# Optimization experiments

Hardware: AMD Instinct MI355X
Metric: run time of the kernel (lower is better)

Reference implementation:

```python
import jax, jax.numpy as jnp
import numpy as np

NH, NKV, HD, PD = 16, 4, 128, 16  # heads, kv heads, head dim, rotary partial dim
BASE = 10000.0
QK_GAIN_INIT = 5.25


def _rms_norm(x):
    # F.rms_norm over last dim, eps = dtype eps (torch default when eps=None)
    return x * jax.lax.rsqrt(jnp.mean(x * x, axis=-1, keepdims=True) + jnp.finfo(x.dtype).eps)


def _rope_partial(x, cos, sin):
    # rotate first PD dims (two halves of PD//2), pass through the rest
    h = PD // 2
    x1, x2, xp = x[..., :h], x[..., h:PD], x[..., PD:]
    return jnp.concatenate([x1 * cos + x2 * sin, -x2 * cos + x1 * sin, xp], axis=-1)


def setup_inputs() -> dict:
    key = jax.random.key(0)
    ks = jax.random.split(key, 5)
    B, T, D = 2, 2048, 2048
    KD = NKV * HD
    s = 0.02
    return {
        "x": jax.random.normal(ks[0], (B, T, D), jnp.float32),
        "wq": jax.random.normal(ks[1], (D, D), jnp.float32) * s,
        "wk": jax.random.normal(ks[2], (KD, D), jnp.float32) * s,
        "wv": jax.random.normal(ks[3], (KD, D), jnp.float32) * s,
        "wp": jax.random.normal(ks[4], (D, D), jnp.float32) * s,
        "qg": jnp.full((NH,), QK_GAIN_INIT, jnp.float32),
    }


def reference(x, wq, wk, wv, wp, qg):
    B, T, D = x.shape
    q = (x @ wq.T).reshape(B, T, NH, HD)    # [B,T,NH,HD]
    k = (x @ wk.T).reshape(B, T, NKV, HD)   # [B,T,NKV,HD]
    v = (x @ wv.T).reshape(B, T, NKV, HD)
    q = _rms_norm(q)
    k = _rms_norm(k)
    # partial rotary tables: [T, PD//2] -> broadcast over head dim
    t = jnp.arange(T, dtype=jnp.float32)
    inv = 1.0 / (BASE ** (jnp.arange(0, PD, 2, dtype=jnp.float32) / PD))
    f = t[:, None] * inv[None, :]
    cos, sin = jnp.cos(f)[:, None, :], jnp.sin(f)[:, None, :]  # [T,1,PD//2]
    q = _rope_partial(q, cos, sin)
    k = _rope_partial(k, cos, sin)
    q = q * qg[None, None, :, None]         # learned per-head QK gain
    scale = 1.0 / jnp.sqrt(jnp.float32(HD))
    G = NH // NKV
    qh = q.reshape(B, T, NKV, G, HD)
    scores = jnp.einsum('bqkgd,bskd->bkgqs', qh, k) * scale  # [B,NKV,G,T,T]
    causal = jnp.arange(T)[:, None] >= jnp.arange(T)[None, :]
    scores = jnp.where(causal[None, None, None], scores, -jnp.inf)
    p = jax.nn.softmax(scores, axis=-1)
    y = jnp.einsum('bkgqs,bskd->bqkgd', p, v).reshape(B, T, D)
    return y @ wp.T
```

## Files before the change

### kernel.cpp

```cpp
#include <hip/hip_runtime.h>
#include <hip/hip_bf16.h>

#define B_   2
#define T_   2048
#define D_   2048
#define NH_  16
#define NKV_ 4
#define HD_  128
#define KD_  512
#define BT_  4096

typedef __bf16 bf16x8 __attribute__((ext_vector_type(8)));
typedef float  f32x4  __attribute__((ext_vector_type(4)));
typedef float  f32x16 __attribute__((ext_vector_type(16)));

__device__ __forceinline__ void gload_lds16(const __hip_bfloat16* g, __hip_bfloat16* l) {
    __builtin_amdgcn_global_load_lds(
        (__attribute__((address_space(1))) void*)(g),
        (__attribute__((address_space(3))) void*)(l),
        16, 0, 0);
}

__global__ void f2b_all(const float4* __restrict__ x,  const float4* __restrict__ wq,
                        const float4* __restrict__ wk, const float4* __restrict__ wv,
                        const float4* __restrict__ wp,
                        ushort4* __restrict__ xb,  ushort4* __restrict__ wqb,
                        ushort4* __restrict__ wkb, ushort4* __restrict__ wvb,
                        ushort4* __restrict__ wpb) {
    const int e0 = BT_ * D_ / 4;
    const int e1 = e0 + D_ * D_ / 4;
    const int e2 = e1 + KD_ * D_ / 4;
    const int e3 = e2 + KD_ * D_ / 4;
    const int e4 = e3 + D_ * D_ / 4;
    int idx = blockIdx.x * blockDim.x + threadIdx.x;
    int stride = gridDim.x * blockDim.x;
    for (int j = idx; j < e4; j += stride) {
        const float4* src; ushort4* dst; int off;
        if      (j < e0) { src = x;  dst = xb;  off = j; }
        else if (j < e1) { src = wq; dst = wqb; off = j - e0; }
        else if (j < e2) { src = wk; dst = wkb; off = j - e1; }
        else if (j < e3) { src = wv; dst = wvb; off = j - e2; }
        else             { src = wp; dst = wpb; off = j - e3; }
        float4 v = src[off];
        __hip_bfloat16 a = __float2bfloat16(v.x), b = __float2bfloat16(v.y),
                       c = __float2bfloat16(v.z), d = __float2bfloat16(v.w);
        ushort4 o;
        o.x = *(const unsigned short*)&a; o.y = *(const unsigned short*)&b;
        o.z = *(const unsigned short*)&c; o.w = *(const unsigned short*)&d;
        dst[off] = o;
    }
}

#define GEMM_TILE_BODY(Aptr, Bptr, Cptr, colL, Nc, K)                                         \
    const int tid = threadIdx.x, w = tid >> 6, lane = tid & 63;                               \
    const int lr = lane & 15, lk = lane >> 4;                                                 \
    const int wr = w >> 1, wc = w & 1;                                                        \
    const size_t row0 = (size_t)blockIdx.x * 128;                                             \
    const __hip_bfloat16* ga = (Aptr) + (row0 + tid / 4) * (K) + (tid % 4) * 8;               \
    const __hip_bfloat16* gb = (Bptr) + ((size_t)(colL) + tid / 4) * (K) + (tid % 4) * 8;     \
    const int KI = (K) >> 5;                                                                  \
    auto stage = [&](int u) {                                                                 \
        int uu = u < KI ? u : KI - 1;                                                         \
        const int kk = uu * 32;                                                               \
        const int slot = u & 3;                                                               \
        gload_lds16(ga + kk,                  &As[slot][w * 512]);                            \
        gload_lds16(ga + kk + (size_t)64*(K), &As[slot][2048 + w * 512]);                     \
        gload_lds16(gb + kk,                  &Bs[slot][w * 512]);                            \
        gload_lds16(gb + kk + (size_t)64*(K), &Bs[slot][2048 + w * 512]);                     \
    };                                                                                        \
    f32x4 acc[4][4] = {};                                                                     \
    stage(0); stage(1);                                                                       \
    for (int kt = 0; kt < KI; ++kt) {                                                         \
        stage(kt + 2);                                                                        \
        asm volatile("s_waitcnt vmcnt(8)" ::: "memory");                                      \
        __builtin_amdgcn_s_barrier();                                                         \
        __builtin_amdgcn_sched_barrier(0);                                                    \
        const int slot = kt & 3;                                                              \
        bf16x8 af[4], bfr[4];                                                                 \
        _Pragma("unroll")                                                                     \
        for (int m = 0; m < 4; m++)                                                           \
            af[m] = *(const bf16x8*)&As[slot][(wr * 64 + m * 16 + lr) * 32 + lk * 8];         \
        _Pragma("unroll")                                                                     \
        for (int n = 0; n < 4; n++)                                                           \
            bfr[n] = *(const bf16x8*)&Bs[slot][(wc * 64 + n * 16 + lr) * 32 + lk * 8];        \
        _Pragma("unroll")                                                                     \
        for (int m = 0; m < 4; m++)                                                           \
            _Pragma("unroll")                                                                 \
            for (int n = 0; n < 4; n++)                                                       \
                acc[m][n] = __builtin_amdgcn_mfma_f32_16x16x32_bf16(af[m], bfr[n],            \
                                                                    acc[m][n], 0, 0, 0);      \
    }                                                                                         \
    _Pragma("unroll")                                                                         \
    for (int m = 0; m < 4; m++)                                                               \
        _Pragma("unroll")                                                                     \
        for (int n = 0; n < 4; n++)                                                           \
            _Pragma("unroll")                                                                 \
            for (int r = 0; r < 4; r++)                                                       \
                (Cptr)[(row0 + wr * 64 + m * 16 + lk * 4 + r) * (Nc)                          \
                       + (colL) + wc * 64 + n * 16 + lr] = acc[m][n][r];

__global__ __launch_bounds__(256, 2)
void gemm_qkv(const __hip_bfloat16* __restrict__ A,
              const __hip_bfloat16* __restrict__ Wq, const __hip_bfloat16* __restrict__ Wk,
              const __hip_bfloat16* __restrict__ Wv,
              float* __restrict__ Cq, float* __restrict__ Ck, float* __restrict__ Cv) {
    __shared__ __attribute__((aligned(16))) __hip_bfloat16 As[4][4096];
    __shared__ __attribute__((aligned(16))) __hip_bfloat16 Bs[4][4096];
    const int cb = blockIdx.y;
    const __hip_bfloat16* Bw; float* Cm; int Nc, colL;
    if (cb < 16)      { Bw = Wq; Cm = Cq; Nc = D_;  colL = cb * 128; }
    else if (cb < 20) { Bw = Wk; Cm = Ck; Nc = KD_; colL = (cb - 16) * 128; }
    else              { Bw = Wv; Cm = Cv; Nc = KD_; colL = (cb - 20) * 128; }
    GEMM_TILE_BODY(A, Bw, Cm, colL, Nc, D_)
}

__global__ __launch_bounds__(256, 2)
void gemm_p(const __hip_bfloat16* __restrict__ A, const __hip_bfloat16* __restrict__ B,
            float* __restrict__ C, int N, int K) {
    __shared__ __attribute__((aligned(16))) __hip_bfloat16 As[4][4096];
    __shared__ __attribute__((aligned(16))) __hip_bfloat16 Bs[4][4096];
    const int colL = blockIdx.y * 128;
    GEMM_TILE_BODY(A, B, C, colL, N, K)
}

__global__ __launch_bounds__(256)
void norm_rope(const float* __restrict__ qf, const float* __restrict__ kf, const float* __restrict__ vf,
               const float* __restrict__ qg,
               __hip_bfloat16* __restrict__ qb, __hip_bfloat16* __restrict__ kfb, __hip_bfloat16* __restrict__ vb) {
    int wid  = (blockIdx.x * 256 + threadIdx.x) >> 6;
    int lane = threadIdx.x & 63;
    int bt = wid / 24, hh = wid % 24;
    int b = bt >> 11, t = bt & (T_ - 1);

    const float* row;
    if (hh < NH_)            row = qf + (size_t)bt * D_  + hh * HD_;
    else if (hh < NH_+NKV_)  row = kf + (size_t)bt * KD_ + (hh - NH_) * HD_;
    else                     row = vf + (size_t)bt * KD_ + (hh - NH_ - NKV_) * HD_;

    float2 xv = *(const float2*)(row + lane * 2);

    if (hh >= NH_ + NKV_) {
        int kv = hh - NH_ - NKV_;
        __hip_bfloat16* o = vb + ((size_t)(b * NKV_ + kv) * T_ + t) * HD_ + lane * 2;
        o[0] = __float2bfloat16(xv.x); o[1] = __float2bfloat16(xv.y);
        return;
    }

    float ss = xv.x * xv.x + xv.y * xv.y;
    #pragma unroll
    for (int off = 32; off; off >>= 1) ss += __shfl_xor(ss, off);
    float rn = rsqrtf(ss * (1.0f / HD_) + 1.1920929e-7f);
    float y0 = xv.x * rn, y1 = xv.y * rn;

    float py0 = __shfl_xor(y0, 4), py1 = __shfl_xor(y1, 4);
    float o0 = y0, o1 = y1;
    if (lane < 8) {
        int i0 = (2 * lane) & 7;
        float f0 = (float)t * exp2f(-(float)i0       * 1.66096404744368f);
        float f1 = (float)t * exp2f(-(float)(i0 + 1) * 1.66096404744368f);
        float s0, c0, s1, c1;
        sincosf(f0, &s0, &c0);
        sincosf(f1, &s1, &c1);
        if (lane < 4) { o0 =  y0 * c0 + py0 * s0; o1 =  y1 * c1 + py1 * s1; }
        else          { o0 = -y0 * c0 + py0 * s0; o1 = -y1 * c1 + py1 * s1; }
    }

    if (hh < NH_) {
        float g = qg[hh] * 0.1275174305f;
        o0 *= g; o1 *= g;
        __hip_bfloat16* o = qb + ((size_t)(b * NH_ + hh) * T_ + t) * HD_ + lane * 2;
        o[0] = __float2bfloat16(o0); o[1] = __float2bfloat16(o1);
    } else {
        int kv = hh - NH_;
        int hb  = lane >> 3;
        int hi2 = (lane >> 2) & 1;
        int j   = (2 * lane) & 7;
        size_t idxe = (size_t)(b * NKV_ + kv) * T_ * HD_
                    + (size_t)((((t >> 5) * 8 + hb) * 2 + hi2)) * 256 + (t & 31) * 8 + j;
        __hip_bfloat16* o = kfb + idxe;
        o[0] = __float2bfloat16(o0); o[1] = __float2bfloat16(o1);
    }
}

__global__ void vfrag_k(const __hip_bfloat16* __restrict__ vb, __hip_bfloat16* __restrict__ vfb) {
    __shared__ __hip_bfloat16 tile[32][33];
    int bk = blockIdx.z;
    int t0 = blockIdx.x * 32, d0 = blockIdx.y * 32;
    int tx = threadIdx.x, ty = threadIdx.y;
    const __hip_bfloat16* src = vb + ((size_t)bk * T_ + t0) * HD_ + d0;
    #pragma unroll
    for (int j = 0; j < 4; j++) tile[ty + j * 8][tx] = src[(size_t)(ty + j * 8) * HD_ + tx];
    __syncthreads();
    if (ty < 4) {
        int sect = ty, l31 = tx;
        ushort4 u0, u1;
        unsigned short* up0 = (unsigned short*)&u0;
        unsigned short* up1 = (unsigned short*)&u1;
        #pragma unroll
        for (int j = 0; j < 4; j++) up0[j] = *(const unsigned short*)&tile[sect * 8 + j][l31];
        #pragma unroll
        for (int j = 0; j < 4; j++) up1[j] = *(const unsigned short*)&tile[sect * 8 + 4 + j][l31];
        ushort4* dst = (ushort4*)(vfb + (size_t)bk * T_ * HD_
                     + (size_t)((((blockIdx.x * 4 + blockIdx.y) * 4 + sect) * 32 + l31)) * 8);
        dst[0] = u0; dst[1] = u1;
    }
}

__device__ __forceinline__ unsigned pkbf(float a, float b) {
    __hip_bfloat16 x = __float2bfloat16(a), y = __float2bfloat16(b);
    unsigned short xu = *(const unsigned short*)&x, yu = *(const unsigned short*)&y;
    return (unsigned)xu | ((unsigned)yu << 16);
}

union U8u { unsigned u[4]; bf16x8 v; };

__global__ __launch_bounds__(512, 2)
void attn_fwd(const __hip_bfloat16* __restrict__ qb, const __hip_bfloat16* __restrict__ kfb,
              const __hip_bfloat16* __restrict__ vfb, __hip_bfloat16* __restrict__ yb) {
    __shared__ float Mrg[4][4224];
    const int tid  = threadIdx.x;
    const int w    = tid >> 6, lane = tid & 63;
    const int l31  = lane & 31, hi = lane >> 5;
    const int hd4  = w & 3;
    const int seg  = w >> 2;
    const int bid  = blockIdx.x;
    const int strm = bid & 7;
    const int b    = strm >> 2, kvh = strm & 3;
    const int idx  = bid >> 3;
    const int c    = (idx < 32) ? (63 - 2 * idx) : (126 - 2 * idx);
    const int ns   = (c >> 1) + 1;
    const int h    = kvh * 4 + hd4;
    const int qa   = c * 32;

    const __hip_bfloat16* qp  = qb  + ((size_t)(b * NH_ + h) * T_ + qa) * HD_;
    const __hip_bfloat16* kfp = kfb + (size_t)(b * NKV_ + kvh) * T_ * HD_ + lane * 8;
    const __hip_bfloat16* vfp = vfb + (size_t)(b * NKV_ + kvh) * T_ * HD_ + lane * 8;

    bf16x8 qfr[8];
    #pragma unroll
    for (int hb = 0; hb < 8; ++hb)
        qfr[hb] = *(const bf16x8*)(qp + (size_t)l31 * HD_ + hb * 16 + hi * 8);

    f32x16 o0 = {}, o1 = {}, o2 = {}, o3 = {};
    float m = -1e30f, s = 0.f;

    bf16x8 kk[8], vv[8];
    {
        int kt0 = seg ? (ns <= c ? ns : c) : 0;
        #pragma unroll
        for (int hb = 0; hb < 8; ++hb)
            kk[hb] = *(const bf16x8*)(kfp + ((size_t)kt0 * 16 + hb * 2) * 256);
    }

    for (int t = 0; t < ns; ++t) {
        __builtin_amdgcn_s_barrier();

        const int kt_raw = seg ? ns + t : t;
        const bool dead  = kt_raw > c;
        const int kt     = dead ? c : kt_raw;

        #pragma unroll
        for (int db = 0; db < 4; ++db) {
            vv[db * 2]     = *(const bf16x8*)(vfp + ((size_t)kt * 16 + db * 4) * 256);
            vv[db * 2 + 1] = *(const bf16x8*)(vfp + ((size_t)kt * 16 + db * 4) * 256 + 512);
        }

        f32x16 sa = {};
        __builtin_amdgcn_s_setprio(1);
        #pragma unroll
        for (int hb = 0; hb < 8; ++hb)
            sa = __builtin_amdgcn_mfma_f32_32x32x16_bf16(kk[hb], qfr[hb], sa, 0, 0, 0);
        __builtin_amdgcn_s_setprio(0);

        {
            int ktn_r = (seg ? ns : 0) + t + 1;
            int ktn = ktn_r > c ? c : ktn_r;
            #pragma unroll
            for (int hb = 0; hb < 8; ++hb)
                kk[hb] = *(const bf16x8*)(kfp + ((size_t)ktn * 16 + hb * 2) * 256);
        }

        if (dead) {
            #pragma unroll
            for (int r = 0; r < 16; ++r) sa[r] = -1e30f;
        } else if (kt == c) {
            #pragma unroll
            for (int r = 0; r < 16; ++r) {
                int kvrel = (r & 3) + 8 * (r >> 2) + 4 * hi;
                if (kvrel > l31) sa[r] = -1e30f;
            }
        }
        float pm = sa[0];
        #pragma unroll
        for (int r = 1; r < 16; ++r) pm = fmaxf(pm, sa[r]);
        pm = fmaxf(pm, __shfl_xor(pm, 32));
        if (!__all(pm <= m + 8.f)) {
            float mn = fmaxf(m, pm);
            float corr = exp2f(m - mn);
            s *= corr;
            #pragma unroll
            for (int r = 0; r < 16; ++r) { o0[r] *= corr; o1[r] *= corr; o2[r] *= corr; o3[r] *= corr; }
            m = mn;
        }
        float p[16]; float rs = 0.f;
        #pragma unroll
        for (int r = 0; r < 16; ++r) { p[r] = exp2f(sa[r] - m); rs += p[r]; }
        rs += __shfl_xor(rs, 32);
        s += rs;
        unsigned pk[8];
        #pragma unroll
        for (int jj = 0; jj < 8; ++jj) pk[jj] = pkbf(p[2 * jj], p[2 * jj + 1]);
        unsigned pks[8];
        #pragma unroll
        for (int jj = 0; jj < 8; ++jj) pks[jj] = (unsigned)__shfl_xor((int)pk[jj], 32);
        U8u pa0, pa1;
        pa0.u[0] = hi ? pks[2] : pk[0];
        pa0.u[1] = hi ? pks[3] : pk[1];
        pa0.u[2] = hi ? pk[2]  : pks[0];
        pa0.u[3] = hi ? pk[3]  : pks[1];
        pa1.u[0] = hi ? pks[6] : pk[4];
        pa1.u[1] = hi ? pks[7] : pk[5];
        pa1.u[2] = hi ? pk[6]  : pks[4];
        pa1.u[3] = hi ? pk[7]  : pks[5];
        __builtin_amdgcn_s_setprio(1);
        o0 = __builtin_amdgcn_mfma_f32_32x32x16_bf16(vv[0], pa0.v, o0, 0, 0, 0);
        o0 = __builtin_amdgcn_mfma_f32_32x32x16_bf16(vv[1], pa1.v, o0, 0, 0, 0);
        o1 = __builtin_amdgcn_mfma_f32_32x32x16_bf16(vv[2], pa0.v, o1, 0, 0, 0);
        o1 = __builtin_amdgcn_mfma_f32_32x32x16_bf16(vv[3], pa1.v, o1, 0, 0, 0);
        o2 = __builtin_amdgcn_mfma_f32_32x32x16_bf16(vv[4], pa0.v, o2, 0, 0, 0);
        o2 = __builtin_amdgcn_mfma_f32_32x32x16_bf16(vv[5], pa1.v, o2, 0, 0, 0);
        o3 = __builtin_amdgcn_mfma_f32_32x32x16_bf16(vv[6], pa0.v, o3, 0, 0, 0);
        o3 = __builtin_amdgcn_mfma_f32_32x32x16_bf16(vv[7], pa1.v, o3, 0, 0, 0);
        __builtin_amdgcn_s_setprio(0);
    }

    __syncthreads();
    float* Mh = &Mrg[hd4][0];
    if (seg == 1) {
        #pragma unroll
        for (int r = 0; r < 16; ++r) {
            Mh[(0 * 16 + r) * 64 + lane] = o0[r];
            Mh[(1 * 16 + r) * 64 + lane] = o1[r];
            Mh[(2 * 16 + r) * 64 + lane] = o2[r];
            Mh[(3 * 16 + r) * 64 + lane] = o3[r];
        }
        Mh[4096 + lane] = m;
        Mh[4160 + lane] = s;
    }
    __syncthreads();
    if (seg == 0) {
        float m1 = Mh[4096 + lane], s1 = Mh[4160 + lane];
        float mn = fmaxf(m, m1);
        float ca = exp2f(m - mn), cb = exp2f(m1 - mn);
        s = s * ca + s1 * cb;
        #pragma unroll
        for (int r = 0; r < 16; ++r) {
            o0[r] = o0[r] * ca + Mh[(0 * 16 + r) * 64 + lane] * cb;
            o1[r] = o1[r] * ca + Mh[(1 * 16 + r) * 64 + lane] * cb;
            o2[r] = o2[r] * ca + Mh[(2 * 16 + r) * 64 + lane] * cb;
            o3[r] = o3[r] * ca + Mh[(3 * 16 + r) * 64 + lane] * cb;
        }
        float inv = 1.0f / s;
        __hip_bfloat16* yrow = yb + ((size_t)b * T_ + qa + l31) * D_ + h * HD_;
        #define WRITE_DB(ON, DB)                                                        \
            _Pragma("unroll")                                                           \
            for (int r4 = 0; r4 < 4; ++r4) {                                            \
                ushort4 u;                                                              \
                __hip_bfloat16 e0 = __float2bfloat16(ON[4*r4+0] * inv);                 \
                __hip_bfloat16 e1 = __float2bfloat16(ON[4*r4+1] * inv);                 \
                __hip_bfloat16 e2 = __float2bfloat16(ON[4*r4+2] * inv);                 \
                __hip_bfloat16 e3 = __float2bfloat16(ON[4*r4+3] * inv);                 \
                u.x = *(const unsigned short*)&e0; u.y = *(const unsigned short*)&e1;   \
                u.z = *(const unsigned short*)&e2; u.w = *(const unsigned short*)&e3;   \
                *(ushort4*)(yrow + (DB) * 32 + 8 * r4 + 4 * hi) = u;                    \
            }
        WRITE_DB(o0, 0) WRITE_DB(o1, 1) WRITE_DB(o2, 2) WRITE_DB(o3, 3)
        #undef WRITE_DB
    }
}

extern "C" void kernel_launch(void* const* d_in, const int* in_sizes, int n_in,
                              void* d_out, int out_size, void* d_ws, size_t ws_size,
                              hipStream_t stream) {
    (void)in_sizes; (void)n_in; (void)out_size; (void)ws_size;
    const float* x  = (const float*)d_in[0];
    const float* wq = (const float*)d_in[1];
    const float* wk = (const float*)d_in[2];
    const float* wv = (const float*)d_in[3];
    const float* wp = (const float*)d_in[4];
    const float* qg = (const float*)d_in[5];
    float* out = (float*)d_out;

    char* ws = (char*)d_ws;
    size_t off = 0;
    auto alloc = [&](size_t bytes) { char* p = ws + off; off += (bytes + 255) & ~(size_t)255; return p; };

    __hip_bfloat16* xb  = (__hip_bfloat16*)alloc((size_t)BT_ * D_ * 2);
    __hip_bfloat16* wqb = (__hip_bfloat16*)alloc((size_t)D_ * D_ * 2);
    __hip_bfloat16* wkb = (__hip_bfloat16*)alloc((size_t)KD_ * D_ * 2);
    __hip_bfloat16* wvb = (__hip_bfloat16*)alloc((size_t)KD_ * D_ * 2);
    __hip_bfloat16* wpb = (__hip_bfloat16*)alloc((size_t)D_ * D_ * 2);
    float* qf = (float*)alloc((size_t)BT_ * D_ * 4);
    float* kf = (float*)alloc((size_t)BT_ * KD_ * 4);
    float* vf = (float*)alloc((size_t)BT_ * KD_ * 4);
    __hip_bfloat16* qbb = (__hip_bfloat16*)alloc((size_t)BT_ * D_ * 2);
    __hip_bfloat16* kfb = (__hip_bfloat16*)alloc((size_t)BT_ * KD_ * 2);
    __hip_bfloat16* vfb = (__hip_bfloat16*)alloc((size_t)BT_ * KD_ * 2);
    __hip_bfloat16* ybb = xb;
    __hip_bfloat16* vbb = wqb;

    f2b_all<<<2048, 256, 0, stream>>>((const float4*)x, (const float4*)wq, (const float4*)wk,
                                      (const float4*)wv, (const float4*)wp,
                                      (ushort4*)xb, (ushort4*)wqb, (ushort4*)wkb,
                                      (ushort4*)wvb, (ushort4*)wpb);

    dim3 gqkv(BT_ / 128, 24);
    gemm_qkv<<<gqkv, 256, 0, stream>>>(xb, wqb, wkb, wvb, qf, kf, vf);

    norm_rope<<<(BT_ * 24) / 4, 256, 0, stream>>>(qf, kf, vf, qg, qbb, kfb, vbb);

    dim3 gt(T_ / 32, HD_ / 32, B_ * NKV_);
    vfrag_k<<<gt, dim3(32, 8), 0, stream>>>(vbb, vfb);

    attn_fwd<<<512, 512, 0, stream>>>(qbb, kfb, vfb, ybb);

    dim3 gq(BT_ / 128, D_ / 128);
    gemm_p<<<gq, 256, 0, stream>>>(ybb, wpb, out, D_, D_);
}
```

Before: 236.8 us.

## Split attention KV range four ways per head pair and pair query chunks

```diff
diff --git a/kernel.cpp b/kernel.cpp
--- a/kernel.cpp
+++ b/kernel.cpp
@@ -214,168 +214,183 @@
 
 union U8u { unsigned u[4]; bf16x8 v; };
 
-__global__ __launch_bounds__(512, 2)
+__global__ __launch_bounds__(512, 4)
 void attn_fwd(const __hip_bfloat16* __restrict__ qb, const __hip_bfloat16* __restrict__ kfb,
               const __hip_bfloat16* __restrict__ vfb, __hip_bfloat16* __restrict__ yb) {
-    __shared__ float Mrg[4][4224];
+    __shared__ float Mrg[2][2][4224];
     const int tid  = threadIdx.x;
     const int w    = tid >> 6, lane = tid & 63;
     const int l31  = lane & 31, hi = lane >> 5;
-    const int hd4  = w & 3;
-    const int seg  = w >> 2;
+    const int hsel = w & 1;
+    const int seg  = w >> 1;
     const int bid  = blockIdx.x;
     const int strm = bid & 7;
     const int b    = strm >> 2, kvh = strm & 3;
-    const int idx  = bid >> 3;
-    const int c    = (idx < 32) ? (63 - 2 * idx) : (126 - 2 * idx);
-    const int ns   = (c >> 1) + 1;
-    const int h    = kvh * 4 + hd4;
-    const int qa   = c * 32;
-
-    const __hip_bfloat16* qp  = qb  + ((size_t)(b * NH_ + h) * T_ + qa) * HD_;
+    const int j    = bid >> 3;
+    const int hg   = j & 1, i = j >> 1;
+    const int h    = kvh * 4 + hg * 2 + hsel;
+
     const __hip_bfloat16* kfp = kfb + (size_t)(b * NKV_ + kvh) * T_ * HD_ + lane * 8;
     const __hip_bfloat16* vfp = vfb + (size_t)(b * NKV_ + kvh) * T_ * HD_ + lane * 8;
 
-    bf16x8 qfr[8];
     #pragma unroll
-    for (int hb = 0; hb < 8; ++hb)
-        qfr[hb] = *(const bf16x8*)(qp + (size_t)l31 * HD_ + hb * 16 + hi * 8);
-
-    f32x16 o0 = {}, o1 = {}, o2 = {}, o3 = {};
-    float m = -1e30f, s = 0.f;
-
-    bf16x8 kk[8], vv[8];
-    {
-        int kt0 = seg ? (ns <= c ? ns : c) : 0;
+    for (int phase = 0; phase < 2; ++phase) {
+        const int c  = phase == 0 ? 63 - 2 * i : 2 * i;
+        const int qa = c * 32;
+        const int L  = (c >> 2) + 1;
+
+        const __hip_bfloat16* qp = qb + ((size_t)(b * NH_ + h) * T_ + qa) * HD_;
+        bf16x8 qfr[8];
         #pragma unroll
         for (int hb = 0; hb < 8; ++hb)
-            kk[hb] = *(const bf16x8*)(kfp + ((size_t)kt0 * 16 + hb * 2) * 256);
-    }
-
-    for (int t = 0; t < ns; ++t) {
-        __builtin_amdgcn_s_barrier();
-
-        const int kt_raw = seg ? ns + t : t;
-        const bool dead  = kt_raw > c;
-        const int kt     = dead ? c : kt_raw;
-
-        #pragma unroll
-        for (int db = 0; db < 4; ++db) {
-            vv[db * 2]     = *(const bf16x8*)(vfp + ((size_t)kt * 16 + db * 4) * 256);
-            vv[db * 2 + 1] = *(const bf16x8*)(vfp + ((size_t)kt * 16 + db * 4) * 256 + 512);
+            qfr[hb] = *(const bf16x8*)(qp + (size_t)l31 * HD_ + hb * 16 + hi * 8);
+
+        f32x16 o0 = {}, o1 = {}, o2 = {}, o3 = {};
+        float m = -1e30f, s = 0.f;
+
+        bf16x8 kk[8], vv[8];
+        {
+            int kt0 = seg * L; if (kt0 > c) kt0 = c;
+            #pragma unroll
+            for (int hb = 0; hb < 8; ++hb)
+                kk[hb] = *(const bf16x8*)(kfp + ((size_t)kt0 * 16 + hb * 2) * 256);
         }
 
-        f32x16 sa = {};
-        __builtin_amdgcn_s_setprio(1);
-        #pragma unroll
-        for (int hb = 0; hb < 8; ++hb)
-            sa = __builtin_amdgcn_mfma_f32_32x32x16_bf16(kk[hb], qfr[hb], sa, 0, 0, 0);
-        __builtin_amdgcn_s_setprio(0);
-
-        {
-            int ktn_r = (seg ? ns : 0) + t + 1;
-            int ktn = ktn_r > c ? c : ktn_r;
+        for (int t = 0; t < L; ++t) {
+            const int kt_raw = seg * L + t;
+            const bool dead  = kt_raw > c;
+            const int kt     = dead ? c : kt_raw;
+
+            #pragma unroll
+            for (int db = 0; db < 4; ++db) {
+                vv[db * 2]     = *(const bf16x8*)(vfp + ((size_t)kt * 16 + db * 4) * 256);
+                vv[db * 2 + 1] = *(const bf16x8*)(vfp + ((size_t)kt * 16 + db * 4) * 256 + 512);
+            }
+
+            f32x16 sa = {};
+            __builtin_amdgcn_s_setprio(1);
             #pragma unroll
             for (int hb = 0; hb < 8; ++hb)
-                kk[hb] = *(const bf16x8*)(kfp + ((size_t)ktn * 16 + hb * 2) * 256);
+                sa = __builtin_amdgcn_mfma_f32_32x32x16_bf16(kk[hb], qfr[hb], sa, 0, 0, 0);
+            __builtin_amdgcn_s_setprio(0);
+
+            {
+                int ktn = seg * L + t + 1; if (ktn > c) ktn = c;
+                #pragma unroll
+                for (int hb = 0; hb < 8; ++hb)
+                    kk[hb] = *(const bf16x8*)(kfp + ((size_t)ktn * 16 + hb * 2) * 256);
+            }
+
+            if (dead) {
+                #pragma unroll
+                for (int r = 0; r < 16; ++r) sa[r] = -1e30f;
+            } else if (kt == c) {
+                #pragma unroll
+                for (int r = 0; r < 16; ++r) {
+                    int kvrel = (r & 3) + 8 * (r >> 2) + 4 * hi;
+                    if (kvrel > l31) sa[r] = -1e30f;
+                }
+            }
+            float pm = sa[0];
+            #pragma unroll
+            for (int r = 1; r < 16; ++r) pm = fmaxf(pm, sa[r]);
+            pm = fmaxf(pm, __shfl_xor(pm, 32));
+            if (!__all(pm <= m + 8.f)) {
+                float mn = fmaxf(m, pm);
+                float corr = exp2f(m - mn);
+                s *= corr;
+                #pragma unroll
+                for (int r = 0; r < 16; ++r) { o0[r] *= corr; o1[r] *= corr; o2[r] *= corr; o3[r] *= corr; }
+                m = mn;
+            }
+            float p[16]; float rs = 0.f;
+            #pragma unroll
+            for (int r = 0; r < 16; ++r) { p[r] = exp2f(sa[r] - m); rs += p[r]; }
+            rs += __shfl_xor(rs, 32);
+            s += rs;
+            unsigned pk[8];
+            #pragma unroll
+            for (int jj = 0; jj < 8; ++jj) pk[jj] = pkbf(p[2 * jj], p[2 * jj + 1]);
+            unsigned pks[8];
+            #pragma unroll
+            for (int jj = 0; jj < 8; ++jj) pks[jj] = (unsigned)__shfl_xor((int)pk[jj], 32);
+            U8u pa0, pa1;
+            pa0.u[0] = hi ? pks[2] : pk[0];
+            pa0.u[1] = hi ? pks[3] : pk[1];
+            pa0.u[2] = hi ? pk[2]  : pks[0];
+            pa0.u[3] = hi ? pk[3]  : pks[1];
+            pa1.u[0] = hi ? pks[6] : pk[4];
+            pa1.u[1] = hi ? pks[7] : pk[5];
+            pa1.u[2] = hi ? pk[6]  : pks[4];
+            pa1.u[3] = hi ? pk[7]  : pks[5];
+            __builtin_amdgcn_s_setprio(1);
+            o0 = __builtin_amdgcn_mfma_f32_32x32x16_bf16(vv[0], pa0.v, o0, 0, 0, 0);
+            o0 = __builtin_amdgcn_mfma_f32_32x32x16_bf16(vv[1], pa1.v, o0, 0, 0, 0);
+            o1 = __builtin_amdgcn_mfma_f32_32x32x16_bf16(vv[2], pa0.v, o1, 0, 0, 0);
+            o1 = __builtin_amdgcn_mfma_f32_32x32x16_bf16(vv[3], pa1.v, o1, 0, 0, 0);
+            o2 = __builtin_amdgcn_mfma_f32_32x32x16_bf16(vv[4], pa0.v, o2, 0, 0, 0);
+            o2 = __builtin_amdgcn_mfma_f32_32x32x16_bf16(vv[5], pa1.v, o2, 0, 0, 0);
+            o3 = __builtin_amdgcn_mfma_f32_32x32x16_bf16(vv[6], pa0.v, o3, 0, 0, 0);
+            o3 = __builtin_amdgcn_mfma_f32_32x32x16_bf16(vv[7], pa1.v, o3, 0, 0, 0);
+            __builtin_amdgcn_s_setprio(0);
         }
 
-        if (dead) {
-            #pragma unroll
-            for (int r = 0; r < 16; ++r) sa[r] = -1e30f;
-        } else if (kt == c) {
+        auto writePart = [&](float* R) {
             #pragma unroll
             for (int r = 0; r < 16; ++r) {
-                int kvrel = (r & 3) + 8 * (r >> 2) + 4 * hi;
-                if (kvrel > l31) sa[r] = -1e30f;
-            }
+                R[(r)      * 64 + lane] = o0[r];
+                R[(16 + r) * 64 + lane] = o1[r];
+                R[(32 + r) * 64 + lane] = o2[r];
+                R[(48 + r) * 64 + lane] = o3[r];
+            }
+            R[4096 + lane] = m;
+            R[4160 + lane] = s;
+        };
+        auto mergePart = [&](const float* R) {
+            float m1 = R[4096 + lane], s1 = R[4160 + lane];
+            float mn = fmaxf(m, m1);
+            float ca = exp2f(m - mn), cb = exp2f(m1 - mn);
+            s = s * ca + s1 * cb;
+            #pragma unroll
+            for (int r = 0; r < 16; ++r) {
+                o0[r] = o0[r] * ca + R[(r)      * 64 + lane] * cb;
+                o1[r] = o1[r] * ca + R[(16 + r) * 64 + lane] * cb;
+                o2[r] = o2[r] * ca + R[(32 + r) * 64 + lane] * cb;
+                o3[r] = o3[r] * ca + R[(48 + r) * 64 + lane] * cb;
+            }
+            m = mn;
+        };
+
+        float* R0 = &Mrg[hsel][0][0];
+        float* R1 = &Mrg[hsel][1][0];
+        __syncthreads();
+        if (seg == 1) writePart(R0);
+        if (seg == 3) writePart(R1);
+        __syncthreads();
+        if (seg == 0) mergePart(R0);
+        if (seg == 2) mergePart(R1);
+        __syncthreads();
+        if (seg == 2) writePart(R0);
+        __syncthreads();
+        if (seg == 0) {
+            mergePart(R0);
+            float inv = 1.0f / s;
+            __hip_bfloat16* yrow = yb + ((size_t)b * T_ + qa + l31) * D_ + h * HD_;
+            #define WRITE_DB(ON, DB)                                                        \
+                _Pragma("unroll")                                                           \
+                for (int r4 = 0; r4 < 4; ++r4) {                                            \
+                    ushort4 u;                                                              \
+                    __hip_bfloat16 e0 = __float2bfloat16(ON[4*r4+0] * inv);                 \
+                    __hip_bfloat16 e1 = __float2bfloat16(ON[4*r4+1] * inv);                 \
+                    __hip_bfloat16 e2 = __float2bfloat16(ON[4*r4+2] * inv);                 \
+                    __hip_bfloat16 e3 = __float2bfloat16(ON[4*r4+3] * inv);                 \
+                    u.x = *(const unsigned short*)&e0; u.y = *(const unsigned short*)&e1;   \
+                    u.z = *(const unsigned short*)&e2; u.w = *(const unsigned short*)&e3;   \
+                    *(ushort4*)(yrow + (DB) * 32 + 8 * r4 + 4 * hi) = u;                    \
+                }
+            WRITE_DB(o0, 0) WRITE_DB(o1, 1) WRITE_DB(o2, 2) WRITE_DB(o3, 3)
+            #undef WRITE_DB
         }
-        float pm = sa[0];
-        #pragma unroll
-        for (int r = 1; r < 16; ++r) pm = fmaxf(pm, sa[r]);
-        pm = fmaxf(pm, __shfl_xor(pm, 32));
-        if (!__all(pm <= m + 8.f)) {
-            float mn = fmaxf(m, pm);
-            float corr = exp2f(m - mn);
-            s *= corr;
-            #pragma unroll
-            for (int r = 0; r < 16; ++r) { o0[r] *= corr; o1[r] *= corr; o2[r] *= corr; o3[r] *= corr; }
-            m = mn;
-        }
-        float p[16]; float rs = 0.f;
-        #pragma unroll
-        for (int r = 0; r < 16; ++r) { p[r] = exp2f(sa[r] - m); rs += p[r]; }
-        rs += __shfl_xor(rs, 32);
-        s += rs;
-        unsigned pk[8];
-        #pragma unroll
-        for (int jj = 0; jj < 8; ++jj) pk[jj] = pkbf(p[2 * jj], p[2 * jj + 1]);
-        unsigned pks[8];
-        #pragma unroll
-        for (int jj = 0; jj < 8; ++jj) pks[jj] = (unsigned)__shfl_xor((int)pk[jj], 32);
-        U8u pa0, pa1;
-        pa0.u[0] = hi ? pks[2] : pk[0];
-        pa0.u[1] = hi ? pks[3] : pk[1];
-        pa0.u[2] = hi ? pk[2]  : pks[0];
-        pa0.u[3] = hi ? pk[3]  : pks[1];
-        pa1.u[0] = hi ? pks[6] : pk[4];
-        pa1.u[1] = hi ? pks[7] : pk[5];
-        pa1.u[2] = hi ? pk[6]  : pks[4];
-        pa1.u[3] = hi ? pk[7]  : pks[5];
-        __builtin_amdgcn_s_setprio(1);
-        o0 = __builtin_amdgcn_mfma_f32_32x32x16_bf16(vv[0], pa0.v, o0, 0, 0, 0);
-        o0 = __builtin_amdgcn_mfma_f32_32x32x16_bf16(vv[1], pa1.v, o0, 0, 0, 0);
-        o1 = __builtin_amdgcn_mfma_f32_32x32x16_bf16(vv[2], pa0.v, o1, 0, 0, 0);
-        o1 = __builtin_amdgcn_mfma_f32_32x32x16_bf16(vv[3], pa1.v, o1, 0, 0, 0);
-        o2 = __builtin_amdgcn_mfma_f32_32x32x16_bf16(vv[4], pa0.v, o2, 0, 0, 0);
-        o2 = __builtin_amdgcn_mfma_f32_32x32x16_bf16(vv[5], pa1.v, o2, 0, 0, 0);
-        o3 = __builtin_amdgcn_mfma_f32_32x32x16_bf16(vv[6], pa0.v, o3, 0, 0, 0);
-        o3 = __builtin_amdgcn_mfma_f32_32x32x16_bf16(vv[7], pa1.v, o3, 0, 0, 0);
-        __builtin_amdgcn_s_setprio(0);
-    }
-
-    __syncthreads();
-    float* Mh = &Mrg[hd4][0];
-    if (seg == 1) {
-        #pragma unroll
-        for (int r = 0; r < 16; ++r) {
-            Mh[(0 * 16 + r) * 64 + lane] = o0[r];
-            Mh[(1 * 16 + r) * 64 + lane] = o1[r];
-            Mh[(2 * 16 + r) * 64 + lane] = o2[r];
-            Mh[(3 * 16 + r) * 64 + lane] = o3[r];
-        }
-        Mh[4096 + lane] = m;
-        Mh[4160 + lane] = s;
-    }
-    __syncthreads();
-    if (seg == 0) {
-        float m1 = Mh[4096 + lane], s1 = Mh[4160 + lane];
-        float mn = fmaxf(m, m1);
-        float ca = exp2f(m - mn), cb = exp2f(m1 - mn);
-        s = s * ca + s1 * cb;
-        #pragma unroll
-        for (int r = 0; r < 16; ++r) {
-            o0[r] = o0[r] * ca + Mh[(0 * 16 + r) * 64 + lane] * cb;
-            o1[r] = o1[r] * ca + Mh[(1 * 16 + r) * 64 + lane] * cb;
-            o2[r] = o2[r] * ca + Mh[(2 * 16 + r) * 64 + lane] * cb;
-            o3[r] = o3[r] * ca + Mh[(3 * 16 + r) * 64 + lane] * cb;
-        }
-        float inv = 1.0f / s;
-        __hip_bfloat16* yrow = yb + ((size_t)b * T_ + qa + l31) * D_ + h * HD_;
-        #define WRITE_DB(ON, DB)                                                        \
-            _Pragma("unroll")                                                           \
-            for (int r4 = 0; r4 < 4; ++r4) {                                            \
-                ushort4 u;                                                              \
-                __hip_bfloat16 e0 = __float2bfloat16(ON[4*r4+0] * inv);                 \
-                __hip_bfloat16 e1 = __float2bfloat16(ON[4*r4+1] * inv);                 \
-                __hip_bfloat16 e2 = __float2bfloat16(ON[4*r4+2] * inv);                 \
-                __hip_bfloat16 e3 = __float2bfloat16(ON[4*r4+3] * inv);                 \
-                u.x = *(const unsigned short*)&e0; u.y = *(const unsigned short*)&e1;   \
-                u.z = *(const unsigned short*)&e2; u.w = *(const unsigned short*)&e3;   \
-                *(ushort4*)(yrow + (DB) * 32 + 8 * r4 + 4 * hi) = u;                    \
-            }
-        WRITE_DB(o0, 0) WRITE_DB(o1, 1) WRITE_DB(o2, 2) WRITE_DB(o3, 3)
-        #undef WRITE_DB
     }
 }
 
```

New measurement: 533.6 us. 125% more time.

## Fuse RMS norm, partial RoPE, gain and K/V fragment layout into QKV GEMM epilogue

Applied to the files above, without the earlier changes.

```diff
diff --git a/kernel.cpp b/kernel.cpp
--- a/kernel.cpp
+++ b/kernel.cpp
@@ -51,7 +51,7 @@
     }
 }
 
-#define GEMM_TILE_BODY(Aptr, Bptr, Cptr, colL, Nc, K)                                         \
+#define GEMM_PIPE(Aptr, Bptr, colL, K)                                                        \
     const int tid = threadIdx.x, w = tid >> 6, lane = tid & 63;                               \
     const int lr = lane & 15, lk = lane >> 4;                                                 \
     const int wr = w >> 1, wc = w & 1;                                                        \
@@ -89,121 +89,142 @@
             for (int n = 0; n < 4; n++)                                                       \
                 acc[m][n] = __builtin_amdgcn_mfma_f32_16x16x32_bf16(af[m], bfr[n],            \
                                                                     acc[m][n], 0, 0, 0);      \
-    }                                                                                         \
-    _Pragma("unroll")                                                                         \
-    for (int m = 0; m < 4; m++)                                                               \
-        _Pragma("unroll")                                                                     \
-        for (int n = 0; n < 4; n++)                                                           \
-            _Pragma("unroll")                                                                 \
-            for (int r = 0; r < 4; r++)                                                       \
-                (Cptr)[(row0 + wr * 64 + m * 16 + lk * 4 + r) * (Nc)                          \
-                       + (colL) + wc * 64 + n * 16 + lr] = acc[m][n][r];
-
-__global__ __launch_bounds__(256, 2)
+    }
+
+__global__ __launch_bounds__(256, 3)
 void gemm_qkv(const __hip_bfloat16* __restrict__ A,
               const __hip_bfloat16* __restrict__ Wq, const __hip_bfloat16* __restrict__ Wk,
-              const __hip_bfloat16* __restrict__ Wv,
-              float* __restrict__ Cq, float* __restrict__ Ck, float* __restrict__ Cv) {
+              const __hip_bfloat16* __restrict__ Wv, const float* __restrict__ qg,
+              __hip_bfloat16* __restrict__ qbb, __hip_bfloat16* __restrict__ kfb,
+              __hip_bfloat16* __restrict__ vfb) {
     __shared__ __attribute__((aligned(16))) __hip_bfloat16 As[4][4096];
     __shared__ __attribute__((aligned(16))) __hip_bfloat16 Bs[4][4096];
     const int cb = blockIdx.y;
-    const __hip_bfloat16* Bw; float* Cm; int Nc, colL;
-    if (cb < 16)      { Bw = Wq; Cm = Cq; Nc = D_;  colL = cb * 128; }
-    else if (cb < 20) { Bw = Wk; Cm = Ck; Nc = KD_; colL = (cb - 16) * 128; }
-    else              { Bw = Wv; Cm = Cv; Nc = KD_; colL = (cb - 20) * 128; }
-    GEMM_TILE_BODY(A, Bw, Cm, colL, Nc, D_)
-}
-
-__global__ __launch_bounds__(256, 2)
+    const __hip_bfloat16* Bw;
+    if (cb < 16)      Bw = Wq + (size_t)cb * 128 * D_;
+    else if (cb < 20) Bw = Wk + (size_t)(cb - 16) * 128 * D_;
+    else              Bw = Wv + (size_t)(cb - 20) * 128 * D_;
+
+    GEMM_PIPE(A, Bw, 0, D_)
+
+    asm volatile("s_waitcnt vmcnt(0)" ::: "memory");
+    __syncthreads();
+    float* Red = (float*)&As[0][0];
+
+    if (cb < 20) {
+        float ssp[16];
+        #pragma unroll
+        for (int m = 0; m < 4; m++)
+            #pragma unroll
+            for (int r = 0; r < 4; r++) {
+                float v = 0.f;
+                #pragma unroll
+                for (int n = 0; n < 4; n++) v += acc[m][n][r] * acc[m][n][r];
+                #pragma unroll
+                for (int off = 1; off < 16; off <<= 1) v += __shfl_xor(v, off);
+                ssp[m * 4 + r] = v;
+            }
+        if (lr == 0) {
+            #pragma unroll
+            for (int m = 0; m < 4; m++)
+                #pragma unroll
+                for (int r = 0; r < 4; r++)
+                    Red[wc * 128 + wr * 64 + m * 16 + lk * 4 + r] = ssp[m * 4 + r];
+        }
+        __syncthreads();
+        #pragma unroll
+        for (int m = 0; m < 4; m++)
+            #pragma unroll
+            for (int r = 0; r < 4; r++) {
+                float tot = ssp[m * 4 + r] + Red[(wc ^ 1) * 128 + wr * 64 + m * 16 + lk * 4 + r];
+                float rn = rsqrtf(tot * (1.0f / HD_) + 1.1920929e-7f);
+                #pragma unroll
+                for (int n = 0; n < 4; n++) acc[m][n][r] *= rn;
+            }
+        if (wc == 0) {
+            float invf = exp2f(-(float)(lr & 7) * 1.66096404744368f);
+            #pragma unroll
+            for (int m = 0; m < 4; m++)
+                #pragma unroll
+                for (int r = 0; r < 4; r++) {
+                    int t = (int)((row0 + wr * 64 + m * 16 + lk * 4 + r) & (T_ - 1));
+                    float f = (float)t * invf;
+                    float sn, cs;
+                    sincosf(f, &sn, &cs);
+                    float y  = acc[m][0][r];
+                    float yp = __shfl_xor(y, 8);
+                    acc[m][0][r] = (lr < 8) ? (y * cs + yp * sn) : (-y * cs + yp * sn);
+                }
+        }
+    }
+
+    if (cb < 16) {
+        float g = qg[cb] * 0.1275174305f;
+        #pragma unroll
+        for (int m = 0; m < 4; m++)
+            #pragma unroll
+            for (int r = 0; r < 4; r++) {
+                size_t bt = row0 + wr * 64 + m * 16 + lk * 4 + r;
+                int b = (int)(bt >> 11), t = (int)(bt & (T_ - 1));
+                __hip_bfloat16* dst = qbb + ((size_t)(b * NH_ + cb) * T_ + t) * HD_;
+                #pragma unroll
+                for (int n = 0; n < 4; n++) {
+                    int d = wc * 64 + n * 16 + lr;
+                    dst[d] = __float2bfloat16(acc[m][n][r] * g);
+                }
+            }
+    } else if (cb < 20) {
+        int kv = cb - 16;
+        #pragma unroll
+        for (int m = 0; m < 4; m++)
+            #pragma unroll
+            for (int r = 0; r < 4; r++) {
+                size_t bt = row0 + wr * 64 + m * 16 + lk * 4 + r;
+                int b = (int)(bt >> 11), t = (int)(bt & (T_ - 1));
+                __hip_bfloat16* base = kfb + (size_t)(b * NKV_ + kv) * T_ * HD_;
+                #pragma unroll
+                for (int n = 0; n < 4; n++) {
+                    int d = wc * 64 + n * 16 + lr;
+                    size_t idx = (size_t)((((t >> 5) * 8 + (d >> 4)) * 2 + ((d >> 3) & 1))) * 256
+                               + (t & 31) * 8 + (d & 7);
+                    base[idx] = __float2bfloat16(acc[m][n][r]);
+                }
+            }
+    } else {
+        int kv = cb - 20;
+        #pragma unroll
+        for (int m = 0; m < 4; m++)
+            #pragma unroll
+            for (int r = 0; r < 4; r++) {
+                size_t bt = row0 + wr * 64 + m * 16 + lk * 4 + r;
+                int b = (int)(bt >> 11), t = (int)(bt & (T_ - 1));
+                __hip_bfloat16* base = vfb + (size_t)(b * NKV_ + kv) * T_ * HD_;
+                #pragma unroll
+                for (int n = 0; n < 4; n++) {
+                    int d = wc * 64 + n * 16 + lr;
+                    size_t idx = (size_t)(((((t >> 5) * 4 + (d >> 5)) * 4 + ((t >> 3) & 3)) * 32
+                               + (d & 31))) * 8 + (t & 7);
+                    base[idx] = __float2bfloat16(acc[m][n][r]);
+                }
+            }
+    }
+}
+
+__global__ __launch_bounds__(256, 3)
 void gemm_p(const __hip_bfloat16* __restrict__ A, const __hip_bfloat16* __restrict__ B,
             float* __restrict__ C, int N, int K) {
     __shared__ __attribute__((aligned(16))) __hip_bfloat16 As[4][4096];
     __shared__ __attribute__((aligned(16))) __hip_bfloat16 Bs[4][4096];
     const int colL = blockIdx.y * 128;
-    GEMM_TILE_BODY(A, B, C, colL, N, K)
-}
-
-__global__ __launch_bounds__(256)
-void norm_rope(const float* __restrict__ qf, const float* __restrict__ kf, const float* __restrict__ vf,
-               const float* __restrict__ qg,
-               __hip_bfloat16* __restrict__ qb, __hip_bfloat16* __restrict__ kfb, __hip_bfloat16* __restrict__ vb) {
-    int wid  = (blockIdx.x * 256 + threadIdx.x) >> 6;
-    int lane = threadIdx.x & 63;
-    int bt = wid / 24, hh = wid % 24;
-    int b = bt >> 11, t = bt & (T_ - 1);
-
-    const float* row;
-    if (hh < NH_)            row = qf + (size_t)bt * D_  + hh * HD_;
-    else if (hh < NH_+NKV_)  row = kf + (size_t)bt * KD_ + (hh - NH_) * HD_;
-    else                     row = vf + (size_t)bt * KD_ + (hh - NH_ - NKV_) * HD_;
-
-    float2 xv = *(const float2*)(row + lane * 2);
-
-    if (hh >= NH_ + NKV_) {
-        int kv = hh - NH_ - NKV_;
-        __hip_bfloat16* o = vb + ((size_t)(b * NKV_ + kv) * T_ + t) * HD_ + lane * 2;
-        o[0] = __float2bfloat16(xv.x); o[1] = __float2bfloat16(xv.y);
-        return;
-    }
-
-    float ss = xv.x * xv.x + xv.y * xv.y;
+    GEMM_PIPE(A, B, colL, K)
     #pragma unroll
-    for (int off = 32; off; off >>= 1) ss += __shfl_xor(ss, off);
-    float rn = rsqrtf(ss * (1.0f / HD_) + 1.1920929e-7f);
-    float y0 = xv.x * rn, y1 = xv.y * rn;
-
-    float py0 = __shfl_xor(y0, 4), py1 = __shfl_xor(y1, 4);
-    float o0 = y0, o1 = y1;
-    if (lane < 8) {
-        int i0 = (2 * lane) & 7;
-        float f0 = (float)t * exp2f(-(float)i0       * 1.66096404744368f);
-        float f1 = (float)t * exp2f(-(float)(i0 + 1) * 1.66096404744368f);
-        float s0, c0, s1, c1;
-        sincosf(f0, &s0, &c0);
-        sincosf(f1, &s1, &c1);
-        if (lane < 4) { o0 =  y0 * c0 + py0 * s0; o1 =  y1 * c1 + py1 * s1; }
-        else          { o0 = -y0 * c0 + py0 * s0; o1 = -y1 * c1 + py1 * s1; }
-    }
-
-    if (hh < NH_) {
-        float g = qg[hh] * 0.1275174305f;
-        o0 *= g; o1 *= g;
-        __hip_bfloat16* o = qb + ((size_t)(b * NH_ + hh) * T_ + t) * HD_ + lane * 2;
-        o[0] = __float2bfloat16(o0); o[1] = __float2bfloat16(o1);
-    } else {
-        int kv = hh - NH_;
-        int hb  = lane >> 3;
-        int hi2 = (lane >> 2) & 1;
-        int j   = (2 * lane) & 7;
-        size_t idxe = (size_t)(b * NKV_ + kv) * T_ * HD_
-                    + (size_t)((((t >> 5) * 8 + hb) * 2 + hi2)) * 256 + (t & 31) * 8 + j;
-        __hip_bfloat16* o = kfb + idxe;
-        o[0] = __float2bfloat16(o0); o[1] = __float2bfloat16(o1);
-    }
-}
-
-__global__ void vfrag_k(const __hip_bfloat16* __restrict__ vb, __hip_bfloat16* __restrict__ vfb) {
-    __shared__ __hip_bfloat16 tile[32][33];
-    int bk = blockIdx.z;
-    int t0 = blockIdx.x * 32, d0 = blockIdx.y * 32;
-    int tx = threadIdx.x, ty = threadIdx.y;
-    const __hip_bfloat16* src = vb + ((size_t)bk * T_ + t0) * HD_ + d0;
-    #pragma unroll
-    for (int j = 0; j < 4; j++) tile[ty + j * 8][tx] = src[(size_t)(ty + j * 8) * HD_ + tx];
-    __syncthreads();
-    if (ty < 4) {
-        int sect = ty, l31 = tx;
-        ushort4 u0, u1;
-        unsigned short* up0 = (unsigned short*)&u0;
-        unsigned short* up1 = (unsigned short*)&u1;
-        #pragma unroll
-        for (int j = 0; j < 4; j++) up0[j] = *(const unsigned short*)&tile[sect * 8 + j][l31];
-        #pragma unroll
-        for (int j = 0; j < 4; j++) up1[j] = *(const unsigned short*)&tile[sect * 8 + 4 + j][l31];
-        ushort4* dst = (ushort4*)(vfb + (size_t)bk * T_ * HD_
-                     + (size_t)((((blockIdx.x * 4 + blockIdx.y) * 4 + sect) * 32 + l31)) * 8);
-        dst[0] = u0; dst[1] = u1;
-    }
+    for (int m = 0; m < 4; m++)
+        #pragma unroll
+        for (int n = 0; n < 4; n++)
+            #pragma unroll
+            for (int r = 0; r < 4; r++)
+                C[(row0 + wr * 64 + m * 16 + lk * 4 + r) * (size_t)N
+                  + colL + wc * 64 + n * 16 + lr] = acc[m][n][r];
 }
 
 __device__ __forceinline__ unsigned pkbf(float a, float b) {
@@ -400,14 +421,10 @@
     __hip_bfloat16* wkb = (__hip_bfloat16*)alloc((size_t)KD_ * D_ * 2);
     __hip_bfloat16* wvb = (__hip_bfloat16*)alloc((size_t)KD_ * D_ * 2);
     __hip_bfloat16* wpb = (__hip_bfloat16*)alloc((size_t)D_ * D_ * 2);
-    float* qf = (float*)alloc((size_t)BT_ * D_ * 4);
-    float* kf = (float*)alloc((size_t)BT_ * KD_ * 4);
-    float* vf = (float*)alloc((size_t)BT_ * KD_ * 4);
     __hip_bfloat16* qbb = (__hip_bfloat16*)alloc((size_t)BT_ * D_ * 2);
     __hip_bfloat16* kfb = (__hip_bfloat16*)alloc((size_t)BT_ * KD_ * 2);
     __hip_bfloat16* vfb = (__hip_bfloat16*)alloc((size_t)BT_ * KD_ * 2);
     __hip_bfloat16* ybb = xb;
-    __hip_bfloat16* vbb = wqb;
 
     f2b_all<<<2048, 256, 0, stream>>>((const float4*)x, (const float4*)wq, (const float4*)wk,
                                       (const float4*)wv, (const float4*)wp,
@@ -415,12 +432,7 @@
                                       (ushort4*)wvb, (ushort4*)wpb);
 
     dim3 gqkv(BT_ / 128, 24);
-    gemm_qkv<<<gqkv, 256, 0, stream>>>(xb, wqb, wkb, wvb, qf, kf, vf);
-
-    norm_rope<<<(BT_ * 24) / 4, 256, 0, stream>>>(qf, kf, vf, qg, qbb, kfb, vbb);
-
-    dim3 gt(T_ / 32, HD_ / 32, B_ * NKV_);
-    vfrag_k<<<gt, dim3(32, 8), 0, stream>>>(vbb, vfb);
+    gemm_qkv<<<gqkv, 256, 0, stream>>>(xb, wqb, wkb, wvb, qg, qbb, kfb, vfb);
 
     attn_fwd<<<512, 512, 0, stream>>>(qbb, kfb, vfb, ybb);
 
```

Result: faster. 220.7 us (-6.8%).
